# Performance work log

Measured on AMD Instinct MI355X. Metric: run time of the kernel, lower is better.

## Reference

```python
import jax, jax.numpy as jnp
import numpy as np

B, T, F = 8, 8192, 1024
H, O = 256, 2


def setup_inputs() -> dict:
    key = jax.random.key(0)
    ks = jax.random.split(key, 12)
    s = 0.02
    return {
        "bags": jax.random.normal(ks[0], (B, T, F), dtype=jnp.float32),
        "mask": jnp.zeros((B, T), dtype=bool),
        "W1": jax.random.normal(ks[1], (F, H), dtype=jnp.float32) * s,
        "b1": jnp.zeros((H,), dtype=jnp.float32),
        "Wv": jax.random.normal(ks[2], (H, H), dtype=jnp.float32) * s,
        "bv": jnp.zeros((H,), dtype=jnp.float32),
        "Wu": jax.random.normal(ks[3], (H, H), dtype=jnp.float32) * s,
        "bu": jnp.zeros((H,), dtype=jnp.float32),
        "ww": jax.random.normal(ks[4], (H, 1), dtype=jnp.float32) * s,
        "bw": jnp.zeros((1,), dtype=jnp.float32),
        "Wc": jax.random.normal(ks[5], (H, O), dtype=jnp.float32) * s,
        "bc": jnp.zeros((O,), dtype=jnp.float32),
    }


def reference(bags, mask, W1, b1, Wv, bv, Wu, bu, ww, bw, Wc, bc):
    # Feature projection + ReLU (dropout is identity in eval mode)
    h = jax.nn.relu(jnp.einsum("btf,fh->bth", bags, W1) + b1)  # (B,T,H)
    # Gated attention
    a_v = jnp.tanh(jnp.einsum("bth,hk->btk", h, Wv) + bv)
    a_u = jax.nn.sigmoid(jnp.einsum("bth,hk->btk", h, Wu) + bu)
    attn_logits = (jnp.einsum("bth,ho->bto", a_v * a_u, ww) + bw)[..., 0]  # (B,T)
    attn_logits = jnp.where(mask, -jnp.inf, attn_logits)
    attn = jax.nn.softmax(attn_logits, axis=1)  # (B,T)
    # Weighted aggregation over tiles
    slide_repr = jnp.einsum("bt,bth->bh", attn, h)  # (B,H)
    logits = slide_repr @ Wc + bc  # (B,O)
    return logits
```

## Files before the change

### kernel.cpp

```cpp
#include <hip/hip_runtime.h>
#include <math.h>

#define BB 8
#define TT 8192
#define FF 1024
#define HH 256
#define OO 2
#define MT 64
#define NBLK ((BB*TT)/MT)
#define PBAG (TT/MT)
#define PSTR 260

typedef __attribute__((ext_vector_type(8))) short bf16x8;
typedef __attribute__((ext_vector_type(4))) float f32x4;

__device__ __forceinline__ float b2f(unsigned short s) {
    union { unsigned u; float f; } v; v.u = ((unsigned)s) << 16; return v.f;
}
__device__ __forceinline__ unsigned short f2b(float f) {
    union { float f; unsigned u; } v; v.f = f;
    unsigned u = v.u;
    return (unsigned short)((u + 0x7fffu + ((u >> 16) & 1u)) >> 16);
}

__global__ __launch_bounds__(256)
void mil_prep(const float* __restrict__ W1,
              const float* __restrict__ Wv,
              const float* __restrict__ Wu,
              unsigned short* __restrict__ W1t,
              unsigned short* __restrict__ Wvt,
              unsigned short* __restrict__ Wut) {
    __shared__ unsigned short T[64 * 72];
    const int b = blockIdx.x;
    const int t = threadIdx.x;
    const float* src;
    unsigned short* dst;
    int kt, nt, dstld;
    if (b < 64)      { src = W1; dst = W1t; kt = b >> 2;        nt = b & 3;        dstld = 1024; }
    else if (b < 80) { src = Wv; dst = Wvt; kt = (b - 64) >> 2; nt = (b - 64) & 3; dstld = 256; }
    else             { src = Wu; dst = Wut; kt = (b - 80) >> 2; nt = (b - 80) & 3; dstld = 256; }

#pragma unroll
    for (int i = 0; i < 4; ++i) {
        int f = t + i * 256;
        int r = f >> 4, c = (f & 15) * 4;
        float4 v = *(const float4*)(src + (size_t)(kt * 64 + r) * 256 + nt * 64 + c);
        T[(c + 0) * 72 + r] = f2b(v.x);
        T[(c + 1) * 72 + r] = f2b(v.y);
        T[(c + 2) * 72 + r] = f2b(v.z);
        T[(c + 3) * 72 + r] = f2b(v.w);
    }
    __syncthreads();
#pragma unroll
    for (int i = 0; i < 2; ++i) {
        int f = t + i * 256;
        int r = f >> 3, s = (f & 7) * 8;
        *(uint4*)(dst + (size_t)(nt * 64 + r) * dstld + kt * 64 + s) = *(uint4*)&T[r * 72 + s];
    }
}

__global__ __launch_bounds__(256, 3)
void mil_main(const float* __restrict__ bags,
              const unsigned char* __restrict__ mask,
              const float* __restrict__ b1,
              const float* __restrict__ bv,
              const float* __restrict__ bu,
              const float* __restrict__ ww,
              const float* __restrict__ bwp,
              const unsigned short* __restrict__ W1t,
              const unsigned short* __restrict__ Wvt,
              const unsigned short* __restrict__ Wut,
              float* __restrict__ P) {
    const int tid  = threadIdx.x;
    const int wave = tid >> 6;
    const int lane = tid & 63;
    const int l15  = lane & 15;
    const int quad = lane >> 4;
    const int blk  = blockIdx.x;
    const int row0 = blk * MT;
    const int bag  = blk >> 7;
    const int trow = (blk & 127) * MT;

    __shared__ unsigned short As[MT * 72];
    __shared__ unsigned short Hs[MT * 264];

    const float bwv = bwp[0];

    f32x4 acc[4][4];
#pragma unroll
    for (int mi = 0; mi < 4; ++mi)
#pragma unroll
        for (int ni = 0; ni < 4; ++ni)
            acc[mi][ni] = (f32x4){0.f, 0.f, 0.f, 0.f};

    const float* bagrow = bags + (size_t)row0 * FF;

    float4 pf[4];
    int pr[4], pc[4];
#pragma unroll
    for (int i = 0; i < 4; ++i) {
        int f = tid + i * 256;
        pr[i] = f >> 4;
        pc[i] = (f & 15) * 4;
        pf[i] = *(const float4*)(bagrow + (size_t)pr[i] * FF + pc[i]);
    }

    for (int kb = 0; kb < FF / 64; ++kb) {
        __syncthreads();
#pragma unroll
        for (int i = 0; i < 4; ++i) {
            unsigned p0 = (unsigned)f2b(pf[i].x) | ((unsigned)f2b(pf[i].y) << 16);
            unsigned p1 = (unsigned)f2b(pf[i].z) | ((unsigned)f2b(pf[i].w) << 16);
            *(uint2*)&As[pr[i] * 72 + pc[i]] = make_uint2(p0, p1);
        }
        __syncthreads();
        bf16x8 bfr[2][4];
#pragma unroll
        for (int k0i = 0; k0i < 2; ++k0i)
#pragma unroll
            for (int ni = 0; ni < 4; ++ni)
                bfr[k0i][ni] = *(const bf16x8*)(W1t + (size_t)(wave * 64 + ni * 16 + l15) * 1024
                                                + kb * 64 + k0i * 32 + quad * 8);
        if (kb < FF / 64 - 1) {
#pragma unroll
            for (int i = 0; i < 4; ++i)
                pf[i] = *(const float4*)(bagrow + (size_t)pr[i] * FF + (kb + 1) * 64 + pc[i]);
        }
#pragma unroll
        for (int k0i = 0; k0i < 2; ++k0i) {
            bf16x8 afr[4];
#pragma unroll
            for (int mi = 0; mi < 4; ++mi)
                afr[mi] = *(const bf16x8*)&As[(mi * 16 + l15) * 72 + k0i * 32 + quad * 8];
#pragma unroll
            for (int mi = 0; mi < 4; ++mi)
#pragma unroll
                for (int ni = 0; ni < 4; ++ni)
                    acc[mi][ni] = __builtin_amdgcn_mfma_f32_16x16x32_bf16(afr[mi], bfr[k0i][ni], acc[mi][ni], 0, 0, 0);
        }
    }

    {
        float bb[4];
#pragma unroll
        for (int ni = 0; ni < 4; ++ni) bb[ni] = b1[wave * 64 + ni * 16 + l15];
#pragma unroll
        for (int mi = 0; mi < 4; ++mi)
#pragma unroll
            for (int ni = 0; ni < 4; ++ni) {
                int n = wave * 64 + ni * 16 + l15;
#pragma unroll
                for (int r = 0; r < 4; ++r) {
                    int m = mi * 16 + quad * 4 + r;
                    float h = acc[mi][ni][r] + bb[ni];
                    h = fmaxf(h, 0.f);
                    Hs[m * 264 + n] = f2b(h);
                }
            }
    }
    __syncthreads();

    float* logits = (float*)As;
    float* wrow   = logits + 64;
    float* sc     = wrow + 64;
    if (tid < MT) logits[tid] = 0.f;
    __syncthreads();

    float rsum[4][4];
#pragma unroll
    for (int mi = 0; mi < 4; ++mi)
#pragma unroll
        for (int r = 0; r < 4; ++r) rsum[mi][r] = 0.f;

#pragma unroll
    for (int nc = 0; nc < 2; ++nc) {
        f32x4 av[4][2], au[4][2];
#pragma unroll
        for (int mi = 0; mi < 4; ++mi)
#pragma unroll
            for (int j = 0; j < 2; ++j) {
                av[mi][j] = (f32x4){0.f, 0.f, 0.f, 0.f};
                au[mi][j] = (f32x4){0.f, 0.f, 0.f, 0.f};
            }
#pragma unroll 2
        for (int ks = 0; ks < 8; ++ks) {
            int k = ks * 32 + quad * 8;
            bf16x8 bvf[2], buf[2];
#pragma unroll
            for (int j = 0; j < 2; ++j) {
                int n = wave * 64 + (nc * 2 + j) * 16 + l15;
                bvf[j] = *(const bf16x8*)(Wvt + (size_t)n * 256 + k);
                buf[j] = *(const bf16x8*)(Wut + (size_t)n * 256 + k);
            }
            bf16x8 afr[4];
#pragma unroll
            for (int mi = 0; mi < 4; ++mi)
                afr[mi] = *(const bf16x8*)&Hs[(mi * 16 + l15) * 264 + k];
#pragma unroll
            for (int mi = 0; mi < 4; ++mi)
#pragma unroll
                for (int j = 0; j < 2; ++j) {
                    av[mi][j] = __builtin_amdgcn_mfma_f32_16x16x32_bf16(afr[mi], bvf[j], av[mi][j], 0, 0, 0);
                    au[mi][j] = __builtin_amdgcn_mfma_f32_16x16x32_bf16(afr[mi], buf[j], au[mi][j], 0, 0, 0);
                }
        }
#pragma unroll
        for (int j = 0; j < 2; ++j) {
            int n = wave * 64 + (nc * 2 + j) * 16 + l15;
            float bvn = bv[n], bun = bu[n], wn = ww[n];
#pragma unroll
            for (int mi = 0; mi < 4; ++mi)
#pragma unroll
                for (int r = 0; r < 4; ++r) {
                    float tv = tanhf(av[mi][j][r] + bvn);
                    float su = 1.f / (1.f + expf(-(au[mi][j][r] + bun)));
                    rsum[mi][r] += tv * su * wn;
                }
        }
    }
#pragma unroll
    for (int mi = 0; mi < 4; ++mi)
#pragma unroll
        for (int r = 0; r < 4; ++r) {
            float s = rsum[mi][r];
            s += __shfl_xor(s, 1);
            s += __shfl_xor(s, 2);
            s += __shfl_xor(s, 4);
            s += __shfl_xor(s, 8);
            if (l15 == 0) atomicAdd(&logits[mi * 16 + quad * 4 + r], s);
        }
    __syncthreads();

    if (tid < MT) {
        float lg = logits[tid] + bwv;
        if (mask[bag * TT + trow + tid]) lg = -INFINITY;
        logits[tid] = lg;
    }
    __syncthreads();

    if (wave == 0) {
        float v = logits[lane];
        float mx = v;
#pragma unroll
        for (int off = 1; off < 64; off <<= 1) mx = fmaxf(mx, __shfl_xor(mx, off));
        float w = (mx == -INFINITY) ? 0.f : expf(v - mx);
        wrow[lane] = w;
        float l = w;
#pragma unroll
        for (int off = 1; off < 64; off <<= 1) l += __shfl_xor(l, off);
        if (lane == 0) { sc[0] = mx; sc[1] = l; }
    }
    __syncthreads();

    float a = 0.f;
#pragma unroll 8
    for (int m = 0; m < MT; ++m)
        a += wrow[m] * b2f(Hs[m * 264 + tid]);

    float* rec = P + (size_t)blk * PSTR;
    rec[2 + tid] = a;
    if (tid == 0) { rec[0] = sc[0]; rec[1] = sc[1]; }
}

__global__ void mil_final(const float* __restrict__ P,
                          const float* __restrict__ Wc,
                          const float* __restrict__ bc,
                          float* __restrict__ out) {
    const int bag = blockIdx.x;
    const int tid = threadIdx.x;
    __shared__ float marr[PBAG];
    __shared__ float earr[PBAG];
    __shared__ float red[4];
    __shared__ float wred[8];

    if (tid < PBAG) marr[tid] = P[(size_t)(bag * PBAG + tid) * PSTR + 0];
    __syncthreads();
    if (tid < PBAG) {
        float v = marr[tid];
#pragma unroll
        for (int off = 1; off < 64; off <<= 1) v = fmaxf(v, __shfl_xor(v, off));
        if ((tid & 63) == 0) red[tid >> 6] = v;
    }
    __syncthreads();
    const float M = fmaxf(red[0], red[1]);
    if (tid < PBAG) {
        float e = (marr[tid] == -INFINITY) ? 0.f : expf(marr[tid] - M);
        earr[tid] = e;
        float le = P[(size_t)(bag * PBAG + tid) * PSTR + 1] * e;
#pragma unroll
        for (int off = 1; off < 64; off <<= 1) le += __shfl_xor(le, off);
        if ((tid & 63) == 0) red[2 + (tid >> 6)] = le;
    }
    __syncthreads();
    const float L = red[2] + red[3];

    float accv = 0.f;
    for (int i = 0; i < PBAG; ++i)
        accv += earr[i] * P[(size_t)(bag * PBAG + i) * PSTR + 2 + tid];
    const float sr = accv / L;

    float p0 = sr * Wc[tid * 2 + 0];
    float p1 = sr * Wc[tid * 2 + 1];
#pragma unroll
    for (int off = 1; off < 64; off <<= 1) {
        p0 += __shfl_xor(p0, off);
        p1 += __shfl_xor(p1, off);
    }
    if ((tid & 63) == 0) {
        wred[(tid >> 6) * 2 + 0] = p0;
        wred[(tid >> 6) * 2 + 1] = p1;
    }
    __syncthreads();
    if (tid == 0) {
        out[bag * 2 + 0] = wred[0] + wred[2] + wred[4] + wred[6] + bc[0];
        out[bag * 2 + 1] = wred[1] + wred[3] + wred[5] + wred[7] + bc[1];
    }
}

extern "C" void kernel_launch(void* const* d_in, const int* in_sizes, int n_in,
                              void* d_out, int out_size, void* d_ws, size_t ws_size,
                              hipStream_t stream) {
    const float*         bags = (const float*)d_in[0];
    const unsigned char* mask = (const unsigned char*)d_in[1];
    const float*         W1   = (const float*)d_in[2];
    const float*         b1   = (const float*)d_in[3];
    const float*         Wv   = (const float*)d_in[4];
    const float*         bv   = (const float*)d_in[5];
    const float*         Wu   = (const float*)d_in[6];
    const float*         bu   = (const float*)d_in[7];
    const float*         ww   = (const float*)d_in[8];
    const float*         bw   = (const float*)d_in[9];
    const float*         Wc   = (const float*)d_in[10];
    const float*         bc   = (const float*)d_in[11];
    float* out = (float*)d_out;

    char* ws = (char*)d_ws;
    unsigned short* W1t = (unsigned short*)(ws);
    unsigned short* Wvt = (unsigned short*)(ws + 524288);
    unsigned short* Wut = (unsigned short*)(ws + 655360);
    float*          P   = (float*)(ws + 786432);

    mil_prep<<<96, 256, 0, stream>>>(W1, Wv, Wu, W1t, Wvt, Wut);
    mil_main<<<NBLK, 256, 0, stream>>>(bags, mask, b1, bv, bu, ww, bw, W1t, Wvt, Wut, P);
    mil_final<<<BB, 256, 0, stream>>>(P, Wc, bc, out);
}
```

Baseline: 496.7 us.

## Load bag tiles directly into MFMA registers, drop LDS staging, use fast exp

The first GEMM no longer stages fp32 bag tiles through shared memory. Each lane loads its A fragment straight from global memory, converts it to bf16 in registers, and double-buffers both the A and W1 fragments across 32 k-steps, which removes two barriers per k-block. The gated-attention loop is restructured to one 16-column chunk at a time, and tanh, sigmoid and the softmax exponentials use fast __expf/__frcp_rn forms. Occupancy is lowered to 2 blocks per SM to leave room for the extra registers. The direct global loads are less coalesced (16 rows by 32 bytes per instruction) and lower occupancy may expose memory latency.

```diff
diff --git a/kernel.cpp b/kernel.cpp
--- a/kernel.cpp
+++ b/kernel.cpp
@@ -21,6 +21,9 @@
     union { float f; unsigned u; } v; v.f = f;
     unsigned u = v.u;
     return (unsigned short)((u + 0x7fffu + ((u >> 16) & 1u)) >> 16);
+}
+__device__ __forceinline__ unsigned pk2(float a, float b) {
+    return (unsigned)f2b(a) | ((unsigned)f2b(b) << 16);
 }
 
 __global__ __launch_bounds__(256)
@@ -59,7 +62,7 @@
     }
 }
 
-__global__ __launch_bounds__(256, 3)
+__global__ __launch_bounds__(256, 2)
 void mil_main(const float* __restrict__ bags,
               const unsigned char* __restrict__ mask,
               const float* __restrict__ b1,
@@ -81,8 +84,10 @@
     const int bag  = blk >> 7;
     const int trow = (blk & 127) * MT;
 
-    __shared__ unsigned short As[MT * 72];
     __shared__ unsigned short Hs[MT * 264];
+    __shared__ float logits[MT];
+    __shared__ float wrow[MT];
+    __shared__ float sc[2];
 
     const float bwv = bwp[0];
 
@@ -94,50 +99,57 @@
             acc[mi][ni] = (f32x4){0.f, 0.f, 0.f, 0.f};
 
     const float* bagrow = bags + (size_t)row0 * FF;
-
-    float4 pf[4];
-    int pr[4], pc[4];
-#pragma unroll
-    for (int i = 0; i < 4; ++i) {
-        int f = tid + i * 256;
-        pr[i] = f >> 4;
-        pc[i] = (f & 15) * 4;
-        pf[i] = *(const float4*)(bagrow + (size_t)pr[i] * FF + pc[i]);
-    }
-
-    for (int kb = 0; kb < FF / 64; ++kb) {
-        __syncthreads();
-#pragma unroll
-        for (int i = 0; i < 4; ++i) {
-            unsigned p0 = (unsigned)f2b(pf[i].x) | ((unsigned)f2b(pf[i].y) << 16);
-            unsigned p1 = (unsigned)f2b(pf[i].z) | ((unsigned)f2b(pf[i].w) << 16);
-            *(uint2*)&As[pr[i] * 72 + pc[i]] = make_uint2(p0, p1);
-        }
-        __syncthreads();
-        bf16x8 bfr[2][4];
-#pragma unroll
-        for (int k0i = 0; k0i < 2; ++k0i)
+    const float* aptr[4];
+#pragma unroll
+    for (int mi = 0; mi < 4; ++mi)
+        aptr[mi] = bagrow + (size_t)(mi * 16 + l15) * FF + quad * 8;
+    const unsigned short* bptr[4];
+#pragma unroll
+    for (int ni = 0; ni < 4; ++ni)
+        bptr[ni] = W1t + (size_t)(wave * 64 + ni * 16 + l15) * 1024 + quad * 8;
+
+    float4 abuf[2][4][2];
+    bf16x8 bbuf[2][4];
+#pragma unroll
+    for (int p = 0; p < 2; ++p) {
+#pragma unroll
+        for (int mi = 0; mi < 4; ++mi) {
+            abuf[p][mi][0] = *(const float4*)(aptr[mi] + p * 32);
+            abuf[p][mi][1] = *(const float4*)(aptr[mi] + p * 32 + 4);
+        }
+#pragma unroll
+        for (int ni = 0; ni < 4; ++ni)
+            bbuf[p][ni] = *(const bf16x8*)(bptr[ni] + p * 32);
+    }
+
+#pragma unroll 4
+    for (int s = 0; s < 32; ++s) {
+        const int cur = s & 1;
+        const int sn = (s + 2 < 32) ? (s + 2) : 31;
+        bf16x8 afr[4];
+#pragma unroll
+        for (int mi = 0; mi < 4; ++mi) {
+            float4 x = abuf[cur][mi][0], y = abuf[cur][mi][1];
+            union { bf16x8 v; unsigned u[4]; } t;
+            t.u[0] = pk2(x.x, x.y);
+            t.u[1] = pk2(x.z, x.w);
+            t.u[2] = pk2(y.x, y.y);
+            t.u[3] = pk2(y.z, y.w);
+            afr[mi] = t.v;
+        }
+#pragma unroll
+        for (int mi = 0; mi < 4; ++mi) {
+            abuf[cur][mi][0] = *(const float4*)(aptr[mi] + sn * 32);
+            abuf[cur][mi][1] = *(const float4*)(aptr[mi] + sn * 32 + 4);
+        }
+#pragma unroll
+        for (int mi = 0; mi < 4; ++mi)
 #pragma unroll
             for (int ni = 0; ni < 4; ++ni)
-                bfr[k0i][ni] = *(const bf16x8*)(W1t + (size_t)(wave * 64 + ni * 16 + l15) * 1024
-                                                + kb * 64 + k0i * 32 + quad * 8);
-        if (kb < FF / 64 - 1) {
-#pragma unroll
-            for (int i = 0; i < 4; ++i)
-                pf[i] = *(const float4*)(bagrow + (size_t)pr[i] * FF + (kb + 1) * 64 + pc[i]);
-        }
-#pragma unroll
-        for (int k0i = 0; k0i < 2; ++k0i) {
-            bf16x8 afr[4];
-#pragma unroll
-            for (int mi = 0; mi < 4; ++mi)
-                afr[mi] = *(const bf16x8*)&As[(mi * 16 + l15) * 72 + k0i * 32 + quad * 8];
-#pragma unroll
-            for (int mi = 0; mi < 4; ++mi)
-#pragma unroll
-                for (int ni = 0; ni < 4; ++ni)
-                    acc[mi][ni] = __builtin_amdgcn_mfma_f32_16x16x32_bf16(afr[mi], bfr[k0i][ni], acc[mi][ni], 0, 0, 0);
-        }
+                acc[mi][ni] = __builtin_amdgcn_mfma_f32_16x16x32_bf16(afr[mi], bbuf[cur][ni], acc[mi][ni], 0, 0, 0);
+#pragma unroll
+        for (int ni = 0; ni < 4; ++ni)
+            bbuf[cur][ni] = *(const bf16x8*)(bptr[ni] + sn * 32);
     }
 
     {
@@ -158,11 +170,6 @@
                 }
             }
     }
-    __syncthreads();
-
-    float* logits = (float*)As;
-    float* wrow   = logits + 64;
-    float* sc     = wrow + 64;
     if (tid < MT) logits[tid] = 0.f;
     __syncthreads();
 
@@ -172,51 +179,42 @@
 #pragma unroll
         for (int r = 0; r < 4; ++r) rsum[mi][r] = 0.f;
 
-#pragma unroll
-    for (int nc = 0; nc < 2; ++nc) {
-        f32x4 av[4][2], au[4][2];
+#pragma unroll 1
+    for (int nc = 0; nc < 4; ++nc) {
+        const int n = wave * 64 + nc * 16 + l15;
+        const unsigned short* vp = Wvt + (size_t)n * 256 + quad * 8;
+        const unsigned short* up = Wut + (size_t)n * 256 + quad * 8;
+        f32x4 av[4], au[4];
+#pragma unroll
+        for (int mi = 0; mi < 4; ++mi) {
+            av[mi] = (f32x4){0.f, 0.f, 0.f, 0.f};
+            au[mi] = (f32x4){0.f, 0.f, 0.f, 0.f};
+        }
+#pragma unroll
+        for (int ks = 0; ks < 8; ++ks) {
+            bf16x8 bvf = *(const bf16x8*)(vp + ks * 32);
+            bf16x8 buf = *(const bf16x8*)(up + ks * 32);
+            bf16x8 afr[4];
+#pragma unroll
+            for (int mi = 0; mi < 4; ++mi)
+                afr[mi] = *(const bf16x8*)&Hs[(mi * 16 + l15) * 264 + ks * 32 + quad * 8];
+#pragma unroll
+            for (int mi = 0; mi < 4; ++mi) {
+                av[mi] = __builtin_amdgcn_mfma_f32_16x16x32_bf16(afr[mi], bvf, av[mi], 0, 0, 0);
+                au[mi] = __builtin_amdgcn_mfma_f32_16x16x32_bf16(afr[mi], buf, au[mi], 0, 0, 0);
+            }
+        }
+        const float bvn = bv[n], bun = bu[n], wn = ww[n];
 #pragma unroll
         for (int mi = 0; mi < 4; ++mi)
 #pragma unroll
-            for (int j = 0; j < 2; ++j) {
-                av[mi][j] = (f32x4){0.f, 0.f, 0.f, 0.f};
-                au[mi][j] = (f32x4){0.f, 0.f, 0.f, 0.f};
+            for (int r = 0; r < 4; ++r) {
+                float xv = av[mi][r] + bvn;
+                float xu = au[mi][r] + bun;
+                float tv = 2.f * __frcp_rn(1.f + __expf(-2.f * xv)) - 1.f;
+                float su = __frcp_rn(1.f + __expf(-xu));
+                rsum[mi][r] += tv * su * wn;
             }
-#pragma unroll 2
-        for (int ks = 0; ks < 8; ++ks) {
-            int k = ks * 32 + quad * 8;
-            bf16x8 bvf[2], buf[2];
-#pragma unroll
-            for (int j = 0; j < 2; ++j) {
-                int n = wave * 64 + (nc * 2 + j) * 16 + l15;
-                bvf[j] = *(const bf16x8*)(Wvt + (size_t)n * 256 + k);
-                buf[j] = *(const bf16x8*)(Wut + (size_t)n * 256 + k);
-            }
-            bf16x8 afr[4];
-#pragma unroll
-            for (int mi = 0; mi < 4; ++mi)
-                afr[mi] = *(const bf16x8*)&Hs[(mi * 16 + l15) * 264 + k];
-#pragma unroll
-            for (int mi = 0; mi < 4; ++mi)
-#pragma unroll
-                for (int j = 0; j < 2; ++j) {
-                    av[mi][j] = __builtin_amdgcn_mfma_f32_16x16x32_bf16(afr[mi], bvf[j], av[mi][j], 0, 0, 0);
-                    au[mi][j] = __builtin_amdgcn_mfma_f32_16x16x32_bf16(afr[mi], buf[j], au[mi][j], 0, 0, 0);
-                }
-        }
-#pragma unroll
-        for (int j = 0; j < 2; ++j) {
-            int n = wave * 64 + (nc * 2 + j) * 16 + l15;
-            float bvn = bv[n], bun = bu[n], wn = ww[n];
-#pragma unroll
-            for (int mi = 0; mi < 4; ++mi)
-#pragma unroll
-                for (int r = 0; r < 4; ++r) {
-                    float tv = tanhf(av[mi][j][r] + bvn);
-                    float su = 1.f / (1.f + expf(-(au[mi][j][r] + bun)));
-                    rsum[mi][r] += tv * su * wn;
-                }
-        }
     }
 #pragma unroll
     for (int mi = 0; mi < 4; ++mi)
@@ -243,7 +241,7 @@
         float mx = v;
 #pragma unroll
         for (int off = 1; off < 64; off <<= 1) mx = fmaxf(mx, __shfl_xor(mx, off));
-        float w = (mx == -INFINITY) ? 0.f : expf(v - mx);
+        float w = (mx == -INFINITY) ? 0.f : __expf(v - mx);
         wrow[lane] = w;
         float l = w;
 #pragma unroll
@@ -284,7 +282,7 @@
     __syncthreads();
     const float M = fmaxf(red[0], red[1]);
     if (tid < PBAG) {
-        float e = (marr[tid] == -INFINITY) ? 0.f : expf(marr[tid] - M);
+        float e = (marr[tid] == -INFINITY) ? 0.f : __expf(marr[tid] - M);
         earr[tid] = e;
         float le = P[(size_t)(bag * PBAG + tid) * PSTR + 1] * e;
 #pragma unroll
@@ -295,6 +293,7 @@
     const float L = red[2] + red[3];
 
     float accv = 0.f;
+#pragma unroll 4
     for (int i = 0; i < PBAG; ++i)
         accv += earr[i] * P[(size_t)(bag * PBAG + i) * PSTR + 2 + tid];
     const float sr = accv / L;
```

Result: slower. 546.3 us (+10.0%).
